# Performance work log

Hardware: AMD Instinct MI355X
Metric: run time of the kernel (lower is better)

The kernel has to match this reference:

```python
import jax, jax.numpy as jnp
import numpy as np

U, I, D, E = 50000, 100000, 64, 4000000
N = U + I
N_LAYERS = 3


def setup_inputs() -> dict:
    key = jax.random.key(0)
    k1, k2, k3, k4, k5 = jax.random.split(key, 5)
    user_emb = jax.random.normal(k1, (U, D), dtype=jnp.float32) * 0.1
    item_emb = jax.random.normal(k2, (I, D), dtype=jnp.float32) * 0.1
    edge_rows = jax.random.randint(k3, (E,), 0, N, dtype=jnp.int32)
    edge_cols = jax.random.randint(k4, (E,), 0, N, dtype=jnp.int32)
    # normalized-Laplacian-like positive values
    edge_vals = jax.random.uniform(k5, (E,), dtype=jnp.float32) * 0.01
    return {"user_emb": user_emb, "item_emb": item_emb,
            "edge_rows": edge_rows, "edge_cols": edge_cols,
            "edge_vals": edge_vals}


def _spmm(rows, cols, vals, x):
    # y[r] = sum_{e: rows[e]==r} vals[e] * x[cols[e]]   (COO SpMM)
    gathered = x[cols] * vals[:, None]          # [E, D]
    return jax.ops.segment_sum(gathered, rows, num_segments=N)


def reference(user_emb, item_emb, edge_rows, edge_cols, edge_vals):
    ego = jnp.concatenate([user_emb, item_emb], axis=0)  # [N, D]
    acc = ego
    for _ in range(N_LAYERS):
        ego = _spmm(edge_rows, edge_cols, edge_vals, ego)
        acc = acc + ego
    all_emb = acc / jnp.float32(N_LAYERS + 1)  # mean over stacked layer outputs
    return all_emb[:U], all_emb[U:]
```

## Files before the change

### kernel.cpp

```cpp
#include <hip/hip_runtime.h>
#include <hip/hip_fp16.h>

#define U_CNT 50000
#define I_CNT 100000
#define DIM 64
#define E_CNT 4000000
#define N_CNT (U_CNT + I_CNT)

#define BROWS 512
#define NBUK ((N_CNT + BROWS - 1) / BROWS)
#define CAP  16384
#define CHUNK_A 8192
#define NBLK_A ((E_CNT + CHUNK_A - 1) / CHUNK_A)
#define EPT (CHUNK_A / 512)

typedef unsigned long long u64;
typedef unsigned int u32;
typedef unsigned short u16;
typedef _Float16 f16x2 __attribute__((ext_vector_type(2)));

__device__ __forceinline__ u16 f2h(float f) {
    return __half_as_ushort(__float2half(f));
}
__device__ __forceinline__ float h2f(u16 h) {
    return __half2float(__ushort_as_half(h));
}

__global__ __launch_bounds__(256) void init_kernel(
    const float* __restrict__ user_emb,
    const float* __restrict__ item_emb,
    u16* __restrict__ ego)
{
    long idx = (long)blockIdx.x * blockDim.x + threadIdx.x;
    const long total = (long)N_CNT * DIM / 4;
    if (idx >= total) return;
    long f = idx * 4;
    const long ubound = (long)U_CNT * DIM;
    float4 v;
    if (f < ubound) v = *(const float4*)(user_emb + f);
    else            v = *(const float4*)(item_emb + (f - ubound));
    ushort4 b;
    b.x = f2h(v.x); b.y = f2h(v.y); b.z = f2h(v.z); b.w = f2h(v.w);
    *(ushort4*)(ego + f) = b;
}

__global__ __launch_bounds__(512) void bucket_scatter(
    const int* __restrict__ rows, const int* __restrict__ cols,
    const float* __restrict__ vals, int* __restrict__ bucket_cursor,
    u64* __restrict__ pck1)
{
    __shared__ int hist[NBUK];
    __shared__ int base[NBUK];
    const int tid = threadIdx.x;
    if (tid < NBUK) hist[tid] = 0;
    __syncthreads();

    long e0 = (long)blockIdx.x * CHUNK_A;
    long e1 = e0 + CHUNK_A; if (e1 > E_CNT) e1 = E_CNT;

    u32 saved[EPT];
    int n = 0;
    for (long e = e0 + tid; e < e1; e += 512) {
        int r = rows[e];
        int b = r >> 9;
        int k = atomicAdd(&hist[b], 1);
        saved[n++] = ((u32)b << 22) | ((u32)(r & (BROWS - 1)) << 13) | (u32)k;
    }
    __syncthreads();

    if (tid < NBUK) {
        int h = hist[tid];
        base[tid] = h ? atomicAdd(&bucket_cursor[tid], h) : 0;
    }
    __syncthreads();

    n = 0;
    for (long e = e0 + tid; e < e1; e += 512) {
        u32 s = saved[n++];
        int b  = (int)(s >> 22);
        int rl = (int)((s >> 13) & (BROWS - 1));
        int k  = (int)(s & 8191);
        int pos = base[b] + k;
        if (pos < CAP) {
            u32 vcode = ((u32)f2h(vals[e]) >> 1) & 0x3FFFu;
            u64 packed = ((u64)vcode << 27) | ((u64)(u32)rl << 18) | (u32)cols[e];
            pck1[(long)b * CAP + pos] = packed;
        }
    }
}

__global__ __launch_bounds__(1024) void bucket_scan(
    const int* __restrict__ bucket_cursor, int* __restrict__ bucket_base)
{
    __shared__ int sm[1024];
    int tid = threadIdx.x;
    int c = (tid < NBUK) ? bucket_cursor[tid] : 0;
    int v = (c > CAP) ? CAP : c;
    sm[tid] = v;
    __syncthreads();
    for (int off = 1; off < 1024; off <<= 1) {
        int t = (tid >= off) ? sm[tid - off] : 0;
        __syncthreads();
        sm[tid] += t;
        __syncthreads();
    }
    if (tid < NBUK) bucket_base[tid] = sm[tid] - v;
}

__global__ __launch_bounds__(512) void bucket_sort(
    const u64* __restrict__ pck1,
    const int* __restrict__ bucket_cursor,
    const int* __restrict__ bucket_base,
    u32* __restrict__ pck,
    int* __restrict__ row_start)
{
    __shared__ int h[BROWS];
    __shared__ int sm[BROWS];
    __shared__ int cur[BROWS];
    const int b   = blockIdx.x;
    const int tid = threadIdx.x;
    int cnt = bucket_cursor[b]; if (cnt > CAP) cnt = CAP;
    const int S = bucket_base[b];
    const u64* src = pck1 + (long)b * CAP;

    h[tid] = 0;
    __syncthreads();
    for (int i = tid; i < cnt; i += 512)
        atomicAdd(&h[(int)((src[i] >> 18) & (BROWS - 1))], 1);
    __syncthreads();

    int v = h[tid];
    sm[tid] = v;
    __syncthreads();
    for (int off = 1; off < BROWS; off <<= 1) {
        int t = (tid >= off) ? sm[tid - off] : 0;
        __syncthreads();
        sm[tid] += t;
        __syncthreads();
    }
    int excl = sm[tid] - v;
    cur[tid] = excl;
    int idx = (b << 9) + tid;
    if (idx <= N_CNT) row_start[idx] = S + excl;
    __syncthreads();

    for (int i = tid; i < cnt; i += 512) {
        u64 pv = src[i];
        int rl = (int)((pv >> 18) & (BROWS - 1));
        int p = atomicAdd(&cur[rl], 1);
        pck[S + p] = (u32)(((pv >> 27) << 18) | (pv & 0x3FFFFu));
    }
}

__global__ __launch_bounds__(256) void spmm_csr(
    const int* __restrict__ row_start,
    const u32* __restrict__ pck,
    const u16* __restrict__ x,
    u16* __restrict__ y,
    float* __restrict__ outacc,
    int mode)
{
    const int lane = threadIdx.x & 63;
    const int g    = lane >> 3;
    const int h    = lane & 7;
    int w = (int)(((long)blockIdx.x * blockDim.x + threadIdx.x) >> 6);
    if (w >= N_CNT / 2) return;
    const int r0 = w << 1;
    int s0  = row_start[r0];
    int mid = row_start[r0 + 1];
    int e1  = row_start[r0 + 2];

    const f16x2 Hz = {(_Float16)0, (_Float16)0};
    f16x2 H0 = Hz, H1 = Hz, H2 = Hz, H3 = Hz;
    f16x2 K0 = Hz, K1 = Hz, K2 = Hz, K3 = Hz;

    const int ll = lane & 31;
    int base0 = s0, base1 = mid;

#define GATHER(P) (*(const uint4*)(x + ((long)((P) & 0x3FFFFu) << 6) + (h << 3)))
#define VH(P) __builtin_bit_cast(f16x2, (u32)((((P) >> 17) & 0x7FFEu) * 0x10001u))
#define FMA4(XB, VHV, Q0, Q1, Q2, Q3)                                       \
        Q0 += __builtin_bit_cast(f16x2, (XB).x) * (VHV);                     \
        Q1 += __builtin_bit_cast(f16x2, (XB).y) * (VHV);                     \
        Q2 += __builtin_bit_cast(f16x2, (XB).z) * (VHV);                     \
        Q3 += __builtin_bit_cast(f16x2, (XB).w) * (VHV);

    while (base0 < mid || base1 < e1) {
        int  idx = (lane < 32) ? (base0 + ll) : (base1 + ll);
        int  lim = (lane < 32) ? mid : e1;
        u32 pk = 0u;
        if (idx < lim) pk = __builtin_nontemporal_load(pck + idx);

        u32 p00 = (u32)__shfl((int)pk,      g);
        u32 p01 = (u32)__shfl((int)pk,  8 + g);
        u32 p02 = (u32)__shfl((int)pk, 16 + g);
        u32 p03 = (u32)__shfl((int)pk, 24 + g);
        u32 p10 = (u32)__shfl((int)pk, 32 + g);
        u32 p11 = (u32)__shfl((int)pk, 40 + g);
        u32 p12 = (u32)__shfl((int)pk, 48 + g);
        u32 p13 = (u32)__shfl((int)pk, 56 + g);

        const uint4 xa0 = GATHER(p00);
        const uint4 xa1 = GATHER(p01);
        const uint4 xa2 = GATHER(p02);
        const uint4 xa3 = GATHER(p03);
        const uint4 xb0 = GATHER(p10);
        const uint4 xb1 = GATHER(p11);
        const uint4 xb2 = GATHER(p12);
        const uint4 xb3 = GATHER(p13);

        FMA4(xa0, VH(p00), H0, H1, H2, H3)
        FMA4(xa1, VH(p01), H0, H1, H2, H3)
        FMA4(xa2, VH(p02), H0, H1, H2, H3)
        FMA4(xa3, VH(p03), H0, H1, H2, H3)
        FMA4(xb0, VH(p10), K0, K1, K2, K3)
        FMA4(xb1, VH(p11), K0, K1, K2, K3)
        FMA4(xb2, VH(p12), K0, K1, K2, K3)
        FMA4(xb3, VH(p13), K0, K1, K2, K3)

        base0 += 32; base1 += 32;
        if (base0 > mid) base0 = mid;
        if (base1 > e1)  base1 = e1;
    }
#undef FMA4
#undef VH
#undef GATHER

    #pragma unroll
    for (int off = 8; off < 64; off <<= 1) {
        H0 += __builtin_bit_cast(f16x2, (u32)__shfl_xor((int)__builtin_bit_cast(u32, H0), off));
        H1 += __builtin_bit_cast(f16x2, (u32)__shfl_xor((int)__builtin_bit_cast(u32, H1), off));
        H2 += __builtin_bit_cast(f16x2, (u32)__shfl_xor((int)__builtin_bit_cast(u32, H2), off));
        H3 += __builtin_bit_cast(f16x2, (u32)__shfl_xor((int)__builtin_bit_cast(u32, H3), off));
        K0 += __builtin_bit_cast(f16x2, (u32)__shfl_xor((int)__builtin_bit_cast(u32, K0), off));
        K1 += __builtin_bit_cast(f16x2, (u32)__shfl_xor((int)__builtin_bit_cast(u32, K1), off));
        K2 += __builtin_bit_cast(f16x2, (u32)__shfl_xor((int)__builtin_bit_cast(u32, K2), off));
        K3 += __builtin_bit_cast(f16x2, (u32)__shfl_xor((int)__builtin_bit_cast(u32, K3), off));
    }

    float a0 = g ? (float)K0.x : (float)H0.x, a1 = g ? (float)K0.y : (float)H0.y;
    float a2 = g ? (float)K1.x : (float)H1.x, a3 = g ? (float)K1.y : (float)H1.y;
    float a4 = g ? (float)K2.x : (float)H2.x, a5 = g ? (float)K2.y : (float)H2.y;
    float a6 = g ? (float)K3.x : (float)H3.x, a7 = g ? (float)K3.y : (float)H3.y;

    if (g < 2) {
        long o = ((long)(r0 + g) << 6) + (h << 3);
        if (mode < 2) {
            ushort4 y0, y1;
            y0.x = f2h(a0); y0.y = f2h(a1); y0.z = f2h(a2); y0.w = f2h(a3);
            y1.x = f2h(a4); y1.y = f2h(a5); y1.z = f2h(a6); y1.w = f2h(a7);
            *(ushort4*)(y + o)     = y0;
            *(ushort4*)(y + o + 4) = y1;
        }
        if (mode != 1) {
            const ushort4 xl = *(const ushort4*)(x + o);
            const ushort4 xh = *(const ushort4*)(x + o + 4);
            float o0 = h2f(xl.x), o1 = h2f(xl.y), o2 = h2f(xl.z), o3 = h2f(xl.w);
            float o4 = h2f(xh.x), o5 = h2f(xh.y), o6 = h2f(xh.z), o7 = h2f(xh.w);
            float4 t0, t1;
            if (mode == 0) {
                t0.x = o0 + a0; t0.y = o1 + a1; t0.z = o2 + a2; t0.w = o3 + a3;
                t1.x = o4 + a4; t1.y = o5 + a5; t1.z = o6 + a6; t1.w = o7 + a7;
            } else {
                t0 = *(const float4*)(outacc + o);
                t1 = *(const float4*)(outacc + o + 4);
                t0.x = (t0.x + o0 + a0) * 0.25f; t0.y = (t0.y + o1 + a1) * 0.25f;
                t0.z = (t0.z + o2 + a2) * 0.25f; t0.w = (t0.w + o3 + a3) * 0.25f;
                t1.x = (t1.x + o4 + a4) * 0.25f; t1.y = (t1.y + o5 + a5) * 0.25f;
                t1.z = (t1.z + o6 + a6) * 0.25f; t1.w = (t1.w + o7 + a7) * 0.25f;
            }
            *(float4*)(outacc + o)     = t0;
            *(float4*)(outacc + o + 4) = t1;
        }
    }
}

extern "C" void kernel_launch(void* const* d_in, const int* in_sizes, int n_in,
                              void* d_out, int out_size, void* d_ws, size_t ws_size,
                              hipStream_t stream) {
    const float* user_emb = (const float*)d_in[0];
    const float* item_emb = (const float*)d_in[1];
    const int*   rows     = (const int*)d_in[2];
    const int*   cols     = (const int*)d_in[3];
    const float* vals     = (const float*)d_in[4];
    float* outacc = (float*)d_out;

    char* ws = (char*)d_ws;
    u32*  pck  = (u32*)ws;                        ws += (size_t)E_CNT * 4;
    u64*  pck1 = (u64*)ws;
    u16*  ego  = (u16*)ws;
    u16*  nxt  = ego + (size_t)N_CNT * DIM;
    {
        size_t a = (size_t)NBUK * CAP * 8;
        size_t b = (size_t)N_CNT * DIM * 2 * 2;
        ws += (a > b) ? a : b;
    }
    int* row_start     = (int*)ws;                ws += (size_t)(N_CNT + 16) * 4;
    int* bucket_cursor = (int*)ws;                ws += 1024 * 4;
    int* bucket_base   = (int*)ws;                ws += 1024 * 4;

    hipMemsetAsync(bucket_cursor, 0, (size_t)NBUK * 4, stream);

    bucket_scatter<<<NBLK_A, 512, 0, stream>>>(rows, cols, vals, bucket_cursor, pck1);
    bucket_scan<<<1, 1024, 0, stream>>>(bucket_cursor, bucket_base);
    bucket_sort<<<NBUK, 512, 0, stream>>>(pck1, bucket_cursor, bucket_base, pck, row_start);

    const long total_f4 = (long)N_CNT * DIM / 4;
    const int  vgrid = (int)((total_f4 + 255) / 256);
    init_kernel<<<vgrid, 256, 0, stream>>>(user_emb, item_emb, ego);

    const int spmm_grid = ((N_CNT / 2) * 64 + 255) / 256;
    spmm_csr<<<spmm_grid, 256, 0, stream>>>(row_start, pck, ego, nxt, outacc, 0);
    spmm_csr<<<spmm_grid, 256, 0, stream>>>(row_start, pck, nxt, ego, outacc, 1);
    spmm_csr<<<spmm_grid, 256, 0, stream>>>(row_start, pck, ego, nxt, outacc, 2);
}
```

Before: 316.8 us.

## Stage bucket-scatter entries in LDS sorted by bucket for coalesced global writes

The scatter kernel now runs a block-wide prefix scan over the bucket histogram, places each packed edge into a shared-memory staging buffer ordered by bucket, then writes the staged entries out in order so consecutive threads store to contiguous positions within each bucket. This replaces scattered 8-byte stores to random buckets with mostly coalesced runs. In exchange it uses 64KB of LDS per block for staging, which lowers occupancy, and adds a scan with many barriers.

```diff
diff --git a/kernel.cpp b/kernel.cpp
--- a/kernel.cpp
+++ b/kernel.cpp
@@ -50,13 +50,17 @@
     u64* __restrict__ pck1)
 {
     __shared__ int hist[NBUK];
-    __shared__ int base[NBUK];
+    __shared__ int excl[NBUK];
+    __shared__ int gbase[NBUK];
+    __shared__ int sm[512];
+    __shared__ u64 stg[CHUNK_A];
     const int tid = threadIdx.x;
     if (tid < NBUK) hist[tid] = 0;
     __syncthreads();
 
     long e0 = (long)blockIdx.x * CHUNK_A;
     long e1 = e0 + CHUNK_A; if (e1 > E_CNT) e1 = E_CNT;
+    const int cnt_total = (int)(e1 - e0);
 
     u32 saved[EPT];
     int n = 0;
@@ -68,9 +72,20 @@
     }
     __syncthreads();
 
-    if (tid < NBUK) {
-        int h = hist[tid];
-        base[tid] = h ? atomicAdd(&bucket_cursor[tid], h) : 0;
+    {
+        int v = (tid < NBUK) ? hist[tid] : 0;
+        sm[tid] = v;
+        __syncthreads();
+        for (int off = 1; off < 512; off <<= 1) {
+            int t = (tid >= off) ? sm[tid - off] : 0;
+            __syncthreads();
+            sm[tid] += t;
+            __syncthreads();
+        }
+        if (tid < NBUK) {
+            excl[tid]  = sm[tid] - v;
+            gbase[tid] = v ? atomicAdd(&bucket_cursor[tid], v) : 0;
+        }
     }
     __syncthreads();
 
@@ -80,12 +95,19 @@
         int b  = (int)(s >> 22);
         int rl = (int)((s >> 13) & (BROWS - 1));
         int k  = (int)(s & 8191);
-        int pos = base[b] + k;
-        if (pos < CAP) {
-            u32 vcode = ((u32)f2h(vals[e]) >> 1) & 0x3FFFu;
-            u64 packed = ((u64)vcode << 27) | ((u64)(u32)rl << 18) | (u32)cols[e];
-            pck1[(long)b * CAP + pos] = packed;
-        }
+        u32 vcode = ((u32)f2h(vals[e]) >> 1) & 0x3FFFu;
+        u64 entry = ((u64)(u32)b << 41) | ((u64)vcode << 27)
+                  | ((u64)(u32)rl << 18) | (u32)cols[e];
+        stg[excl[b] + k] = entry;
+    }
+    __syncthreads();
+
+    for (int i = tid; i < cnt_total; i += 512) {
+        u64 v = stg[i];
+        int b = (int)(v >> 41);
+        int pos = gbase[b] + (i - excl[b]);
+        if (pos < CAP)
+            pck1[(long)b * CAP + pos] = v & ((1ULL << 41) - 1);
     }
 }
 
```

Result: faster. 305.1 us (-3.7%).
